# Kernel tuning notes

Hardware: AMD Instinct MI355X
Metric: run time of the kernel (lower is better)

Reference implementation:

```python
import jax, jax.numpy as jnp
import numpy as np

D = 1024
H = 16
HD = D // H  # 64

def setup_inputs() -> dict:
    key = jax.random.key(0)
    ks = jax.random.split(key, 7)
    B, S = 2, 2048
    x = jax.random.normal(ks[0], (B, S, D), dtype=jnp.float32)
    M = jax.random.randint(ks[1], (B, S, S), 0, 2, dtype=jnp.int32)
    s = 1.0 / np.sqrt(D)
    W_q = jax.random.normal(ks[2], (D, D), dtype=jnp.float32) * s
    W_k = jax.random.normal(ks[3], (D, D), dtype=jnp.float32) * s
    W_v = jax.random.normal(ks[4], (D, D), dtype=jnp.float32) * s
    W_o = jax.random.normal(ks[5], (D, D), dtype=jnp.float32) * s
    b_o = jax.random.normal(ks[6], (D,), dtype=jnp.float32) * 0.01
    return {"x": x, "M": M, "W_q": W_q, "W_k": W_k, "W_v": W_v, "W_o": W_o, "b_o": b_o}

def reference(x, M, W_q, W_k, W_v, W_o, b_o):
    B, S, _ = x.shape
    scale = HD ** -0.5
    # project and split heads: [B, H, S, HD]
    def heads(W):
        return (x @ W.T).reshape(B, S, H, HD).transpose(0, 2, 1, 3)
    Q, K, V = heads(W_q), heads(W_k), heads(W_v)
    scores = jnp.einsum('bhqd,bhkd->bhqk', Q, K) * scale
    mask = (M[:, None, :, :] == 0)  # broadcast over heads
    scores = jnp.where(mask, jnp.float32(-1e9), scores)
    A = jax.nn.softmax(scores, axis=-1)
    out = jnp.einsum('bhqk,bhkd->bhqd', A, V)
    out = out.transpose(0, 2, 1, 3).reshape(B, S, D)
    return out @ W_o.T + b_o
```

## Files before the change

### kernel.cpp

```cpp
#include <hip/hip_runtime.h>
#include <hip/hip_bf16.h>

typedef unsigned short u16;
typedef unsigned int u32;
typedef unsigned long long u64;
typedef _Float16 f16;
typedef __attribute__((__ext_vector_type__(4))) _Float16 f16x4;
typedef __attribute__((__ext_vector_type__(8))) short bf16x8;
typedef __attribute__((__ext_vector_type__(4))) float f32x4;
typedef __attribute__((__ext_vector_type__(16))) float f32x16;
typedef __attribute__((__ext_vector_type__(2))) int i32x2;

__device__ __forceinline__ u16 f2bf(float f) {
    u32 u = __float_as_uint(f);
    return (u16)((u + 0x7fffu + ((u >> 16) & 1u)) >> 16);
}

__global__ __launch_bounds__(256) void prep_kernel(
    const float4* __restrict__ x,  const float4* __restrict__ wq,
    const float4* __restrict__ wk, const float4* __restrict__ wv,
    const float4* __restrict__ wo,
    u16* __restrict__ xb, u16* __restrict__ wqb, u16* __restrict__ wkb,
    u16* __restrict__ wvb, u16* __restrict__ wob,
    const int* __restrict__ M, u64* __restrict__ Mb2)
{
    if (blockIdx.x < 8192) {
        int gid = blockIdx.x * 256 + threadIdx.x;
        const float4* src; u16* dst; int off;
        if (gid < 1048576) { src = x; dst = xb; off = gid; }
        else {
            int g = gid - 1048576;
            int sel = g >> 18;
            off = g & 262143;
            src = sel == 0 ? wq : sel == 1 ? wk : sel == 2 ? wv : wo;
            dst = sel == 0 ? wqb : sel == 1 ? wkb : sel == 2 ? wvb : wob;
        }
        float4 f = src[off];
        ushort4 o;
        o.x = f2bf(f.x); o.y = f2bf(f.y); o.z = f2bf(f.z); o.w = f2bf(f.w);
        ((ushort4*)dst)[off] = o;
    } else {
        int wg   = (blockIdx.x - 8192) * 4 + (threadIdx.x >> 6);
        int lane = threadIdx.x & 63;
        int w = wg & 31;
        int q = (wg >> 5) & 2047;
        int b = wg >> 16;
        size_t base = ((size_t)(b * 2048 + q)) * 2048 + w * 64 + lane;
        u64 bits = __ballot(M[base] != 0);
        if (lane == 0) Mb2[(size_t)(b * 32 + w) * 2048 + q] = bits;
    }
}

template<int MODE, int BN>
__global__ __launch_bounds__(256) void gemm_k(
    const u16* __restrict__ Ag, const u16* __restrict__ Bg,
    u16* __restrict__ Cq, u16* __restrict__ Kfr, u16* __restrict__ Vfr,
    float* __restrict__ Cf, const float* __restrict__ bias)
{
    constexpr int Kd = 1024;
    constexpr int NB = BN / 32;
    __shared__ u16 SM[8192 + BN * 64];
    u16* As0 = SM;
    u16* As1 = SM + 4096;
    u16* Bs0 = SM + 8192;
    u16* Bs1 = SM + 8192 + BN * 32;
    const int tid  = threadIdx.x;
    const int wave = tid >> 6, lane = tid & 63;
    const int quad = lane >> 4, l16 = lane & 15;
    const int n0 = blockIdx.x * BN;
    const int m0 = blockIdx.y * 128;

    const int wm = (wave & 1) * 64, wn = (wave >> 1) * (BN / 2);
    f32x4 acc[4][NB];
    #pragma unroll
    for (int i = 0; i < 4; i++)
        #pragma unroll
        for (int j = 0; j < NB; j++)
            acc[i][j] = (f32x4){0.f, 0.f, 0.f, 0.f};

    const int sr = lane >> 2;
    const int sk = (lane & 3) * 8;
    const int ca0 = wave * 2, ca1 = ca0 + 1;
    const u16* gA0 = Ag + (size_t)(m0 + ca0 * 16 + sr) * Kd + sk;
    const u16* gA1 = Ag + (size_t)(m0 + ca1 * 16 + sr) * Kd + sk;
    const int cb0 = (BN == 128) ? wave * 2 : wave;
    const u16* gB0 = Bg + (size_t)(n0 + cb0 * 16 + sr) * Kd + sk;
    const u16* gB1 = (BN == 128) ? Bg + (size_t)(n0 + (cb0 + 1) * 16 + sr) * Kd + sk : nullptr;

    #define GLL16(gp, lp) __builtin_amdgcn_global_load_lds( \
        (const __attribute__((address_space(1))) void*)(gp), \
        (__attribute__((address_space(3))) void*)(lp), 16, 0, 0)

    for (int k0 = 0; k0 < Kd; k0 += 64) {
        __syncthreads();
        GLL16(gA0 + k0, As0 + ca0 * 512);
        GLL16(gA1 + k0, As0 + ca1 * 512);
        GLL16(gB0 + k0, Bs0 + cb0 * 512);
        if (BN == 128) GLL16(gB1 + k0, Bs0 + (cb0 + 1) * 512);
        GLL16(gA0 + k0 + 32, As1 + ca0 * 512);
        GLL16(gA1 + k0 + 32, As1 + ca1 * 512);
        GLL16(gB0 + k0 + 32, Bs1 + cb0 * 512);
        if (BN == 128) GLL16(gB1 + k0 + 32, Bs1 + (cb0 + 1) * 512);
        __syncthreads();

        #pragma unroll
        for (int kk = 0; kk < 2; kk++) {
            const u16* Ah = kk ? As1 : As0;
            const u16* Bh = kk ? Bs1 : Bs0;
            bf16x8 af[4], bfr[NB];
            #pragma unroll
            for (int mb = 0; mb < 4; mb++)
                af[mb] = *(const bf16x8*)&Ah[(wm + mb * 16 + l16) * 32 + quad * 8];
            #pragma unroll
            for (int nb = 0; nb < NB; nb++)
                bfr[nb] = *(const bf16x8*)&Bh[(wn + nb * 16 + l16) * 32 + quad * 8];
            #pragma unroll
            for (int mb = 0; mb < 4; mb++)
                #pragma unroll
                for (int nb = 0; nb < NB; nb++)
                    acc[mb][nb] = __builtin_amdgcn_mfma_f32_16x16x32_bf16(
                        af[mb], bfr[nb], acc[mb][nb], 0, 0, 0);
        }
    }
    #undef GLL16

    if (MODE == 1) {
        #pragma unroll
        for (int mb = 0; mb < 4; mb++)
            #pragma unroll
            for (int nb = 0; nb < NB; nb++) {
                const int row = m0 + wm + mb * 16 + quad * 4;
                const int col = n0 + wn + nb * 16 + l16;
                #pragma unroll
                for (int r = 0; r < 4; r++)
                    Cf[(size_t)(row + r) * 1024 + col] = acc[mb][nb][r] + bias[col];
            }
        return;
    }

    const int region = n0 >> 10;
    if (region == 0) {
        #pragma unroll
        for (int mb = 0; mb < 4; mb++)
            #pragma unroll
            for (int nb = 0; nb < NB; nb++) {
                const int row = m0 + wm + mb * 16 + quad * 4;
                const int ccol = (n0 & 1023) + wn + nb * 16 + l16;
                #pragma unroll
                for (int r = 0; r < 4; r++)
                    Cq[(size_t)(row + r) * 1024 + ccol] =
                        f2bf(acc[mb][nb][r] * 0.18033688011112042f);
            }
        return;
    }

    const int bb = m0 >> 11;
    const int kt_base = (m0 & 2047) >> 6;
    const int head_base = (n0 & 1023) >> 6;
    u16* dst = (region == 1) ? Kfr : Vfr;
    #pragma unroll
    for (int pass = 0; pass < 2; pass++) {
        __syncthreads();
        #pragma unroll
        for (int mb = 0; mb < 4; mb++) {
            const int rowb = wm + mb * 16 + quad * 4;
            if ((rowb >> 6) != pass) continue;
            #pragma unroll
            for (int nb = 0; nb < NB; nb++) {
                const int ccol = wn + nb * 16 + l16;
                const int h2 = ccol >> 6, dd = ccol & 63;
                if (region == 1) {
                    const int t = dd >> 4, hik = (dd >> 3) & 1, j = dd & 7;
                    #pragma unroll
                    for (int r = 0; r < 4; r++) {
                        const int km = (rowb + r) & 63;
                        const int f = (km >> 5) * 4 + t;
                        const int lanek = hik * 32 + (km & 31);
                        SM[((h2 * 8 + f) * 64 + lanek) * 8 + j] = f2bf(acc[mb][nb][r]);
                    }
                } else {
                    const int kinb = rowb & 63;
                    const int t = kinb >> 4, hiv = (kinb >> 3) & 1, jb = kinb & 7;
                    const int f = (dd >> 5) * 4 + t;
                    const int lanev = hiv * 32 + (dd & 31);
                    ushort4 pk;
                    pk.x = f2bf(acc[mb][nb][0]); pk.y = f2bf(acc[mb][nb][1]);
                    pk.z = f2bf(acc[mb][nb][2]); pk.w = f2bf(acc[mb][nb][3]);
                    *(ushort4*)&SM[((h2 * 8 + f) * 64 + lanev) * 8 + jb] = pk;
                }
            }
        }
        __syncthreads();
        const int h2g = tid >> 7;
        const int inner = (tid & 127) * 32;
        const size_t gbase =
            ((size_t)(bb * 16 + head_base + h2g) * 32 + kt_base + pass) * 4096;
        #pragma unroll
        for (int c = 0; c < 4; c++)
            *(bf16x8*)&dst[gbase + inner + c * 8] =
                *(const bf16x8*)&SM[h2g * 4096 + inner + c * 8];
    }
}

__global__ __launch_bounds__(256) void attn_kernel(
    const u16* __restrict__ Qg, const u16* __restrict__ Kfr, const u16* __restrict__ Vfr,
    const u64* __restrict__ Mb2, f16* __restrict__ Opart, float* __restrict__ Lpart)
{
    const int qt = blockIdx.x >> 2;
    const int kh = blockIdx.x & 3;
    const int h  = blockIdx.y;
    const int b  = blockIdx.z;
    const int tid = threadIdx.x, wave = tid >> 6, lane = tid & 63;
    const int l31 = lane & 31, hi = lane >> 5;

    const int qrow0 = qt * 128 + wave * 32;
    const int bh    = b * 16 + h;

    bf16x8 qf[4];
    {
        const u16* qp = Qg + ((size_t)b * 2048 + qrow0 + l31) * 1024 + h * 64 + hi * 8;
        #pragma unroll
        for (int t = 0; t < 4; t++) qf[t] = *(const bf16x8*)(qp + t * 16);
    }

    const u32 fro = (u32)bh * 131072u + (u32)lane * 8u;

    bf16x8 ones;
    #pragma unroll
    for (int j = 0; j < 8; j++) ones[j] = (short)0x3F80;

    f32x16 oacc0, oacc1, lacc;
    #pragma unroll
    for (int i = 0; i < 16; i++) { oacc0[i] = 0.f; oacc1[i] = 0.f; lacc[i] = 0.f; }

    const int kt0 = kh * 8;
    #pragma unroll 1
    for (int kt = kt0; kt < kt0 + 8; kt++) {
        const u64 mwv = Mb2[(size_t)(b * 32 + kt) * 2048 + qrow0 + l31];
        const u32 mlo = ((u32)mwv) >> (hi * 4);
        const u32 mhi = ((u32)(mwv >> 32)) >> (hi * 4);
        const u32 fb = fro + (u32)kt * 4096u;

        #pragma unroll
        for (int ph = 0; ph < 2; ph++) {
            bf16x8 kf[4], vf[4];
            #pragma unroll
            for (int t = 0; t < 4; t++)
                kf[t] = *(const bf16x8*)(Kfr + fb + (u32)(ph * 4 + t) * 512u);
            vf[0] = *(const bf16x8*)(Vfr + fb + (u32)(2 * ph) * 512u);
            vf[1] = *(const bf16x8*)(Vfr + fb + (u32)(2 * ph + 1) * 512u);
            vf[2] = *(const bf16x8*)(Vfr + fb + (u32)(4 + 2 * ph) * 512u);
            vf[3] = *(const bf16x8*)(Vfr + fb + (u32)(4 + 2 * ph + 1) * 512u);

            const u32 mn = ~(ph ? mhi : mlo);
            f32x16 s;
            #pragma unroll
            for (int reg = 0; reg < 16; reg++) {
                const int kb2 = (reg & 3) + 8 * (reg >> 2);
                s[reg] = __int_as_float(
                    __builtin_amdgcn_sbfe((int)mn, kb2, 1) & (int)0xFF800000);
            }
            #pragma unroll
            for (int t = 0; t < 4; t++)
                s = __builtin_amdgcn_mfma_f32_32x32x16_bf16(kf[t], qf[t], s, 0, 0, 0);

            u32 w[8];
            #pragma unroll
            for (int i = 0; i < 8; i++) {
                const float e0 = __builtin_amdgcn_exp2f(s[2 * i]);
                const float e1 = __builtin_amdgcn_exp2f(s[2 * i + 1]);
                w[i] = __builtin_amdgcn_perm(__float_as_uint(e1),
                                             __float_as_uint(e0), 0x07060302u);
            }

            bf16x8 pb[2];
            #pragma unroll
            for (int fl = 0; fl < 2; fl++) {
                i32x2 p02 = __builtin_amdgcn_permlane32_swap(
                    (int)w[4 * fl + 0], (int)w[4 * fl + 2], false, false);
                i32x2 p13 = __builtin_amdgcn_permlane32_swap(
                    (int)w[4 * fl + 1], (int)w[4 * fl + 3], false, false);
                union { u32 u[4]; bf16x8 v; } fu;
                fu.u[0] = (u32)p02[0];
                fu.u[1] = (u32)p13[0];
                fu.u[2] = (u32)p02[1];
                fu.u[3] = (u32)p13[1];
                pb[fl] = fu.v;
            }

            oacc0 = __builtin_amdgcn_mfma_f32_32x32x16_bf16(vf[0], pb[0], oacc0, 0, 0, 0);
            oacc0 = __builtin_amdgcn_mfma_f32_32x32x16_bf16(vf[1], pb[1], oacc0, 0, 0, 0);
            oacc1 = __builtin_amdgcn_mfma_f32_32x32x16_bf16(vf[2], pb[0], oacc1, 0, 0, 0);
            oacc1 = __builtin_amdgcn_mfma_f32_32x32x16_bf16(vf[3], pb[1], oacc1, 0, 0, 0);
            lacc  = __builtin_amdgcn_mfma_f32_32x32x16_bf16(ones,  pb[0], lacc,  0, 0, 0);
            lacc  = __builtin_amdgcn_mfma_f32_32x32x16_bf16(ones,  pb[1], lacc,  0, 0, 0);
        }
    }

    const size_t obase = ((size_t)(kh * 32 + bh) * 2048 + qrow0 + l31) * 64;
    #pragma unroll
    for (int tile = 0; tile < 2; tile++) {
        #pragma unroll
        for (int g = 0; g < 4; g++) {
            const int d0 = tile * 32 + g * 8 + hi * 4;
            f16x4 pkv;
            #pragma unroll
            for (int r = 0; r < 4; r++) {
                const int reg = g * 4 + r;
                pkv[r] = (f16)(tile == 0 ? oacc0[reg] : oacc1[reg]);
            }
            *(f16x4*)&Opart[obase + d0] = pkv;
        }
    }
    Lpart[(size_t)kh * 65536 + bh * 2048 + qrow0 + l31] = lacc[0];
}

__global__ __launch_bounds__(256) void merge_kernel(
    const f16* __restrict__ Opart, const float* __restrict__ Lpart,
    u16* __restrict__ AO)
{
    const int gid = blockIdx.x * 256 + threadIdx.x;
    const int c4 = gid & 15;
    const int q  = (gid >> 4) & 2047;
    const int bh = gid >> 15;
    const int b  = bh >> 4, h = bh & 15;

    float l = 0.f;
    float s0 = 0.f, s1 = 0.f, s2 = 0.f, s3 = 0.f;
    #pragma unroll
    for (int k = 0; k < 4; k++) {
        const size_t pbase = ((size_t)(k * 32 + bh) * 2048 + q) * 64 + c4 * 4;
        f16x4 o = *(const f16x4*)&Opart[pbase];
        s0 += (float)o[0]; s1 += (float)o[1]; s2 += (float)o[2]; s3 += (float)o[3];
        l += Lpart[(size_t)k * 65536 + bh * 2048 + q];
    }
    const float inv = 1.0f / l;
    ushort4 o;
    o.x = f2bf(s0 * inv); o.y = f2bf(s1 * inv);
    o.z = f2bf(s2 * inv); o.w = f2bf(s3 * inv);
    *(ushort4*)&AO[((size_t)b * 2048 + q) * 1024 + h * 64 + c4 * 4] = o;
}

extern "C" void kernel_launch(void* const* d_in, const int* in_sizes, int n_in,
                              void* d_out, int out_size, void* d_ws, size_t ws_size,
                              hipStream_t stream)
{
    const float* x  = (const float*)d_in[0];
    const int*   Mm = (const int*)d_in[1];
    const float* Wq = (const float*)d_in[2];
    const float* Wk = (const float*)d_in[3];
    const float* Wv = (const float*)d_in[4];
    const float* Wo = (const float*)d_in[5];
    const float* bo = (const float*)d_in[6];
    float* out = (float*)d_out;

    u16* ws  = (u16*)d_ws;
    u16* xb  = ws;
    u16* wqb = xb  + 4194304;
    u16* wkb = wqb + 1048576;
    u16* wvb = wkb + 1048576;
    u16* wob = wvb + 1048576;
    u16* Qb  = wob + 1048576;
    u16* Kfr = Qb  + 4194304;
    u16* Vfr = Kfr + 4194304;
    u16* AOb = Vfr + 4194304;
    u64* Mb2 = (u64*)(AOb + 4194304);
    f16* Opart = (f16*)(Mb2 + 131072);
    float* Lpart = (float*)(Opart + 16777216);

    prep_kernel<<<40960, 256, 0, stream>>>(
        (const float4*)x, (const float4*)Wq, (const float4*)Wk,
        (const float4*)Wv, (const float4*)Wo, xb, wqb, wkb, wvb, wob,
        Mm, Mb2);

    dim3 g1(24, 32, 1);
    gemm_k<0, 128><<<g1, 256, 0, stream>>>(xb, wqb, Qb, Kfr, Vfr, nullptr, nullptr);

    dim3 g2(64, 16, 2);
    attn_kernel<<<g2, 256, 0, stream>>>(Qb, Kfr, Vfr, Mb2, Opart, Lpart);

    merge_kernel<<<4096, 256, 0, stream>>>(Opart, Lpart, AOb);

    dim3 g3(16, 32, 1);
    gemm_k<1, 64><<<g3, 256, 0, stream>>>(AOb, wob, nullptr, nullptr, nullptr,
                                          out, bo);
}
```

Measured before the change: 239.9 us.

## Process two query tiles per wave to reuse K/V fragments, halve key split

Each wave now computes 64 query rows, as two 32-row sub-tiles sharing the same K and V fragment loads, which halves K/V global traffic per query. The key dimension is split two ways instead of four, so the attention grid shrinks to 512 blocks and the merge kernel reads two partials instead of four. This costs more registers per thread (six accumulators plus two Q fragment sets), so launch bounds request 2 blocks per CU, and fewer blocks may reduce occupancy and latency hiding.

```diff
diff --git a/kernel.cpp b/kernel.cpp
--- a/kernel.cpp
+++ b/kernel.cpp
@@ -202,43 +202,48 @@
     }
 }
 
-__global__ __launch_bounds__(256) void attn_kernel(
+__global__ __launch_bounds__(256, 2) void attn_kernel(
     const u16* __restrict__ Qg, const u16* __restrict__ Kfr, const u16* __restrict__ Vfr,
     const u64* __restrict__ Mb2, f16* __restrict__ Opart, float* __restrict__ Lpart)
 {
-    const int qt = blockIdx.x >> 2;
-    const int kh = blockIdx.x & 3;
+    const int qt = blockIdx.x >> 1;
+    const int kh = blockIdx.x & 1;
     const int h  = blockIdx.y;
     const int b  = blockIdx.z;
     const int tid = threadIdx.x, wave = tid >> 6, lane = tid & 63;
     const int l31 = lane & 31, hi = lane >> 5;
 
-    const int qrow0 = qt * 128 + wave * 32;
+    const int qrow0 = qt * 256 + wave * 64;
     const int bh    = b * 16 + h;
 
-    bf16x8 qf[4];
+    bf16x8 qfa[4], qfb[4];
     {
         const u16* qp = Qg + ((size_t)b * 2048 + qrow0 + l31) * 1024 + h * 64 + hi * 8;
         #pragma unroll
-        for (int t = 0; t < 4; t++) qf[t] = *(const bf16x8*)(qp + t * 16);
+        for (int t = 0; t < 4; t++) qfa[t] = *(const bf16x8*)(qp + t * 16);
+        #pragma unroll
+        for (int t = 0; t < 4; t++) qfb[t] = *(const bf16x8*)(qp + 32 * 1024 + t * 16);
     }
 
     const u32 fro = (u32)bh * 131072u + (u32)lane * 8u;
+    const u64* mp = Mb2 + (size_t)(b * 32) * 2048 + qrow0 + l31;
 
     bf16x8 ones;
     #pragma unroll
     for (int j = 0; j < 8; j++) ones[j] = (short)0x3F80;
 
-    f32x16 oacc0, oacc1, lacc;
-    #pragma unroll
-    for (int i = 0; i < 16; i++) { oacc0[i] = 0.f; oacc1[i] = 0.f; lacc[i] = 0.f; }
-
-    const int kt0 = kh * 8;
+    f32x16 oa0, oa1, ob0, ob1, la, lb;
+    #pragma unroll
+    for (int i = 0; i < 16; i++) {
+        oa0[i] = 0.f; oa1[i] = 0.f; ob0[i] = 0.f; ob1[i] = 0.f;
+        la[i] = 0.f;  lb[i] = 0.f;
+    }
+
+    const int kt0 = kh * 16;
     #pragma unroll 1
-    for (int kt = kt0; kt < kt0 + 8; kt++) {
-        const u64 mwv = Mb2[(size_t)(b * 32 + kt) * 2048 + qrow0 + l31];
-        const u32 mlo = ((u32)mwv) >> (hi * 4);
-        const u32 mhi = ((u32)(mwv >> 32)) >> (hi * 4);
+    for (int kt = kt0; kt < kt0 + 16; ++kt) {
+        const u64 mwa = mp[(size_t)kt * 2048];
+        const u64 mwb = mp[(size_t)kt * 2048 + 32];
         const u32 fb = fro + (u32)kt * 4096u;
 
         #pragma unroll
@@ -252,48 +257,69 @@
             vf[2] = *(const bf16x8*)(Vfr + fb + (u32)(4 + 2 * ph) * 512u);
             vf[3] = *(const bf16x8*)(Vfr + fb + (u32)(4 + 2 * ph + 1) * 512u);
 
-            const u32 mn = ~(ph ? mhi : mlo);
-            f32x16 s;
+            const u32 mna = ~((ph ? (u32)(mwa >> 32) : (u32)mwa) >> (hi * 4));
+            const u32 mnb = ~((ph ? (u32)(mwb >> 32) : (u32)mwb) >> (hi * 4));
+            f32x16 sa, sb;
             #pragma unroll
             for (int reg = 0; reg < 16; reg++) {
                 const int kb2 = (reg & 3) + 8 * (reg >> 2);
-                s[reg] = __int_as_float(
-                    __builtin_amdgcn_sbfe((int)mn, kb2, 1) & (int)0xFF800000);
-            }
-            #pragma unroll
-            for (int t = 0; t < 4; t++)
-                s = __builtin_amdgcn_mfma_f32_32x32x16_bf16(kf[t], qf[t], s, 0, 0, 0);
-
-            u32 w[8];
+                sa[reg] = __int_as_float(
+                    __builtin_amdgcn_sbfe((int)mna, kb2, 1) & (int)0xFF800000);
+                sb[reg] = __int_as_float(
+                    __builtin_amdgcn_sbfe((int)mnb, kb2, 1) & (int)0xFF800000);
+            }
+            #pragma unroll
+            for (int t = 0; t < 4; t++) {
+                sa = __builtin_amdgcn_mfma_f32_32x32x16_bf16(kf[t], qfa[t], sa, 0, 0, 0);
+                sb = __builtin_amdgcn_mfma_f32_32x32x16_bf16(kf[t], qfb[t], sb, 0, 0, 0);
+            }
+
+            u32 wa[8], wb[8];
             #pragma unroll
             for (int i = 0; i < 8; i++) {
-                const float e0 = __builtin_amdgcn_exp2f(s[2 * i]);
-                const float e1 = __builtin_amdgcn_exp2f(s[2 * i + 1]);
-                w[i] = __builtin_amdgcn_perm(__float_as_uint(e1),
-                                             __float_as_uint(e0), 0x07060302u);
-            }
-
-            bf16x8 pb[2];
+                const float ea0 = __builtin_amdgcn_exp2f(sa[2 * i]);
+                const float ea1 = __builtin_amdgcn_exp2f(sa[2 * i + 1]);
+                wa[i] = __builtin_amdgcn_perm(__float_as_uint(ea1),
+                                              __float_as_uint(ea0), 0x07060302u);
+                const float eb0 = __builtin_amdgcn_exp2f(sb[2 * i]);
+                const float eb1 = __builtin_amdgcn_exp2f(sb[2 * i + 1]);
+                wb[i] = __builtin_amdgcn_perm(__float_as_uint(eb1),
+                                              __float_as_uint(eb0), 0x07060302u);
+            }
+
+            bf16x8 pba[2], pbb[2];
             #pragma unroll
             for (int fl = 0; fl < 2; fl++) {
-                i32x2 p02 = __builtin_amdgcn_permlane32_swap(
-                    (int)w[4 * fl + 0], (int)w[4 * fl + 2], false, false);
-                i32x2 p13 = __builtin_amdgcn_permlane32_swap(
-                    (int)w[4 * fl + 1], (int)w[4 * fl + 3], false, false);
-                union { u32 u[4]; bf16x8 v; } fu;
-                fu.u[0] = (u32)p02[0];
-                fu.u[1] = (u32)p13[0];
-                fu.u[2] = (u32)p02[1];
-                fu.u[3] = (u32)p13[1];
-                pb[fl] = fu.v;
-            }
-
-            oacc0 = __builtin_amdgcn_mfma_f32_32x32x16_bf16(vf[0], pb[0], oacc0, 0, 0, 0);
-            oacc0 = __builtin_amdgcn_mfma_f32_32x32x16_bf16(vf[1], pb[1], oacc0, 0, 0, 0);
-            oacc1 = __builtin_amdgcn_mfma_f32_32x32x16_bf16(vf[2], pb[0], oacc1, 0, 0, 0);
-            oacc1 = __builtin_amdgcn_mfma_f32_32x32x16_bf16(vf[3], pb[1], oacc1, 0, 0, 0);
-            lacc  = __builtin_amdgcn_mfma_f32_32x32x16_bf16(ones,  pb[0], lacc,  0, 0, 0);
-            lacc  = __builtin_amdgcn_mfma_f32_32x32x16_bf16(ones,  pb[1], lacc,  0, 0, 0);
+                i32x2 a02 = __builtin_amdgcn_permlane32_swap(
+                    (int)wa[4 * fl + 0], (int)wa[4 * fl + 2], false, false);
+                i32x2 a13 = __builtin_amdgcn_permlane32_swap(
+                    (int)wa[4 * fl + 1], (int)wa[4 * fl + 3], false, false);
+                union { u32 u[4]; bf16x8 v; } fa;
+                fa.u[0] = (u32)a02[0]; fa.u[1] = (u32)a13[0];
+                fa.u[2] = (u32)a02[1]; fa.u[3] = (u32)a13[1];
+                pba[fl] = fa.v;
+                i32x2 b02 = __builtin_amdgcn_permlane32_swap(
+                    (int)wb[4 * fl + 0], (int)wb[4 * fl + 2], false, false);
+                i32x2 b13 = __builtin_amdgcn_permlane32_swap(
+                    (int)wb[4 * fl + 1], (int)wb[4 * fl + 3], false, false);
+                union { u32 u[4]; bf16x8 v; } fbu;
+                fbu.u[0] = (u32)b02[0]; fbu.u[1] = (u32)b13[0];
+                fbu.u[2] = (u32)b02[1]; fbu.u[3] = (u32)b13[1];
+                pbb[fl] = fbu.v;
+            }
+
+            oa0 = __builtin_amdgcn_mfma_f32_32x32x16_bf16(vf[0], pba[0], oa0, 0, 0, 0);
+            ob0 = __builtin_amdgcn_mfma_f32_32x32x16_bf16(vf[0], pbb[0], ob0, 0, 0, 0);
+            oa0 = __builtin_amdgcn_mfma_f32_32x32x16_bf16(vf[1], pba[1], oa0, 0, 0, 0);
+            ob0 = __builtin_amdgcn_mfma_f32_32x32x16_bf16(vf[1], pbb[1], ob0, 0, 0, 0);
+            oa1 = __builtin_amdgcn_mfma_f32_32x32x16_bf16(vf[2], pba[0], oa1, 0, 0, 0);
+            ob1 = __builtin_amdgcn_mfma_f32_32x32x16_bf16(vf[2], pbb[0], ob1, 0, 0, 0);
+            oa1 = __builtin_amdgcn_mfma_f32_32x32x16_bf16(vf[3], pba[1], oa1, 0, 0, 0);
+            ob1 = __builtin_amdgcn_mfma_f32_32x32x16_bf16(vf[3], pbb[1], ob1, 0, 0, 0);
+            la  = __builtin_amdgcn_mfma_f32_32x32x16_bf16(ones,  pba[0], la,  0, 0, 0);
+            lb  = __builtin_amdgcn_mfma_f32_32x32x16_bf16(ones,  pbb[0], lb,  0, 0, 0);
+            la  = __builtin_amdgcn_mfma_f32_32x32x16_bf16(ones,  pba[1], la,  0, 0, 0);
+            lb  = __builtin_amdgcn_mfma_f32_32x32x16_bf16(ones,  pbb[1], lb,  0, 0, 0);
         }
     }
 
@@ -303,16 +329,19 @@
         #pragma unroll
         for (int g = 0; g < 4; g++) {
             const int d0 = tile * 32 + g * 8 + hi * 4;
-            f16x4 pkv;
+            f16x4 pka, pkb;
             #pragma unroll
             for (int r = 0; r < 4; r++) {
                 const int reg = g * 4 + r;
-                pkv[r] = (f16)(tile == 0 ? oacc0[reg] : oacc1[reg]);
-            }
-            *(f16x4*)&Opart[obase + d0] = pkv;
+                pka[r] = (f16)(tile == 0 ? oa0[reg] : oa1[reg]);
+                pkb[r] = (f16)(tile == 0 ? ob0[reg] : ob1[reg]);
+            }
+            *(f16x4*)&Opart[obase + d0] = pka;
+            *(f16x4*)&Opart[obase + 32 * 64 + d0] = pkb;
         }
     }
-    Lpart[(size_t)kh * 65536 + bh * 2048 + qrow0 + l31] = lacc[0];
+    Lpart[(size_t)kh * 65536 + bh * 2048 + qrow0 + l31] = la[0];
+    Lpart[(size_t)kh * 65536 + bh * 2048 + qrow0 + 32 + l31] = lb[0];
 }
 
 __global__ __launch_bounds__(256) void merge_kernel(
@@ -328,7 +357,7 @@
     float l = 0.f;
     float s0 = 0.f, s1 = 0.f, s2 = 0.f, s3 = 0.f;
     #pragma unroll
-    for (int k = 0; k < 4; k++) {
+    for (int k = 0; k < 2; k++) {
         const size_t pbase = ((size_t)(k * 32 + bh) * 2048 + q) * 64 + c4 * 4;
         f16x4 o = *(const f16x4*)&Opart[pbase];
         s0 += (float)o[0]; s1 += (float)o[1]; s2 += (float)o[2]; s3 += (float)o[3];
@@ -366,7 +395,7 @@
     u16* AOb = Vfr + 4194304;
     u64* Mb2 = (u64*)(AOb + 4194304);
     f16* Opart = (f16*)(Mb2 + 131072);
-    float* Lpart = (float*)(Opart + 16777216);
+    float* Lpart = (float*)(Opart + 8388608);
 
     prep_kernel<<<40960, 256, 0, stream>>>(
         (const float4*)x, (const float4*)Wq, (const float4*)Wk,
@@ -376,7 +405,7 @@
     dim3 g1(24, 32, 1);
     gemm_k<0, 128><<<g1, 256, 0, stream>>>(xb, wqb, Qb, Kfr, Vfr, nullptr, nullptr);
 
-    dim3 g2(64, 16, 2);
+    dim3 g2(16, 16, 2);
     attn_kernel<<<g2, 256, 0, stream>>>(Qb, Kfr, Vfr, Mb2, Opart, Lpart);
 
     merge_kernel<<<4096, 256, 0, stream>>>(Opart, Lpart, AOb);
```

Result: no change. 235.5 us (-1.8%).
